# Kernel optimization log

Measured on AMD Instinct MI355X. Metric: run time of the kernel, lower is better.

The kernel has to match this reference:

```python
import jax, jax.numpy as jnp
import numpy as np
import math

B, C, F, W, NH = 2, 8, 1024, 512, 8
HD = F // NH


def conv2d(x, w, b):
    # NCHW 3x3 same-padding conv with bias
    y = jax.lax.conv_general_dilated(x, w, (1, 1), [(1, 1), (1, 1)],
                                     dimension_numbers=('NCHW', 'OIHW', 'NCHW'))
    return y + b[None, :, None, None]


def mc_linear(x, w):
    # per-channel linear over the feature (h) axis: (b,c,h,w) x (c,f,h) -> (b,c,f,w)
    return jnp.einsum('bchw,cfh->bcfw', x, w)


def split_heads(t):
    # (b,c,f,w) -> transpose(2,3) -> (b,c,w,f) -> (b,c,w,nh,hd) -> (b,c,nh,w,hd)
    b, c, f, w = t.shape
    return jnp.transpose(t.transpose(0, 1, 3, 2).reshape(b, c, w, NH, HD), (0, 1, 3, 2, 4))


def rotate_queries_or_keys(x):
    # lucidrains-style interleaved rotary over the sequence axis (dim -2)
    d, w = x.shape[-1], x.shape[-2]
    inv_freq = 1.0 / (10000.0 ** (jnp.arange(0, d, 2, dtype=jnp.float32) / d))
    freqs = jnp.arange(w, dtype=jnp.float32)[:, None] * inv_freq[None, :]  # (w, d/2)
    freqs = jnp.repeat(freqs, 2, axis=-1)  # (w, d)
    cos, sin = jnp.cos(freqs), jnp.sin(freqs)
    xp = x.reshape(*x.shape[:-1], d // 2, 2)
    x1, x2 = xp[..., 0], xp[..., 1]
    x_rot = jnp.stack((-x2, x1), axis=-1).reshape(x.shape)
    return x * cos + x_rot * sin


def _forward(x, prev_qk, wq_conv, bq_conv, wq_lin, wk_conv, bk_conv, wk_lin,
             wv_conv, bv_conv, wv_lin, wo_lin):
    b, c, h, w = x.shape
    q = rotate_queries_or_keys(split_heads(mc_linear(conv2d(x, wq_conv, bq_conv), wq_lin)))
    k = rotate_queries_or_keys(split_heads(mc_linear(conv2d(x, wk_conv, bk_conv), wk_lin)))
    v = split_heads(mc_linear(conv2d(x, wv_conv, bv_conv), wv_lin))
    # NOTE: original scales by sqrt(h) == sqrt(features), not sqrt(head_dim)
    qk = jnp.einsum('bcnqd,bcnkd->bcnqk', q, k) / math.sqrt(h) + prev_qk
    a = jnp.einsum('bcnqk,bcnkd->bcnqd', jax.nn.softmax(qk, axis=-1), v)
    a = jnp.transpose(a, (0, 1, 3, 2, 4)).reshape(b, c, w, h).transpose(0, 1, 3, 2)
    out = mc_linear(a, wo_lin)
    return out, qk


def setup_inputs() -> dict:
    key = jax.random.key(0)
    ks = jax.random.split(key, 10)
    s = 0.02
    return {
        'x': jax.random.normal(ks[0], (B, C, F, W), dtype=jnp.float32),
        'prev_qk': jax.random.normal(ks[1], (B, C, NH, W, W), dtype=jnp.float32) * 0.1,
        'wq_conv': jax.random.normal(ks[2], (C, C, 3, 3), dtype=jnp.float32) * s,
        'bq_conv': jnp.zeros((C,), dtype=jnp.float32),
        'wq_lin': jax.random.normal(ks[3], (C, F, F), dtype=jnp.float32) * s,
        'wk_conv': jax.random.normal(ks[4], (C, C, 3, 3), dtype=jnp.float32) * s,
        'bk_conv': jnp.zeros((C,), dtype=jnp.float32),
        'wk_lin': jax.random.normal(ks[5], (C, F, F), dtype=jnp.float32) * s,
        'wv_conv': jax.random.normal(ks[6], (C, C, 3, 3), dtype=jnp.float32) * s,
        'bv_conv': jnp.zeros((C,), dtype=jnp.float32),
        'wv_lin': jax.random.normal(ks[7], (C, F, F), dtype=jnp.float32) * s,
        'wo_lin': jax.random.normal(ks[8], (C, F, F), dtype=jnp.float32) * s,
    }


def reference(x, prev_qk, wq_conv, bq_conv, wq_lin, wk_conv, bk_conv, wk_lin,
              wv_conv, bv_conv, wv_lin, wo_lin):
    return _forward(x, prev_qk, wq_conv, bq_conv, wq_lin, wk_conv, bk_conv, wk_lin,
                    wv_conv, bv_conv, wv_lin, wo_lin)
```

## Files before the change

kernel.cpp:

```cpp
#include <hip/hip_runtime.h>
#include <stdint.h>


typedef float f32x4 __attribute__((ext_vector_type(4)));
typedef short s16x8 __attribute__((ext_vector_type(8)));

__device__ __forceinline__ short f2bf(float f) {
  union { float f; uint32_t u; } v; v.f = f;
  uint32_t r = v.u + 0x7FFFu + ((v.u >> 16) & 1u);
  return (short)(r >> 16);
}

__device__ __forceinline__ void g2l16(const void* g, void* l) {
  __builtin_amdgcn_global_load_lds(
      (const __attribute__((address_space(1))) void*)g,
      (__attribute__((address_space(3))) void*)l, 16, 0, 0);
}

__device__ __forceinline__ void gemm_core(const short* __restrict__ A,
                                          const short* __restrict__ B,
                                          int K, short* sA, short* sB,
                                          f32x4 (*acc)[4]) {
  const int tid = threadIdx.x;
  const int lane = tid & 63;
  const int wv = tid >> 6;
  const int wm = wv >> 1, wn = wv & 1;
  const int q = lane >> 4, cix = lane & 15;

  for (int k0 = 0; k0 < K; k0 += 32) {
    __syncthreads();
#pragma unroll
    for (int i = 0; i < 2; ++i) {
      int seg = wv + 4 * i;
      int m = seg * 16 + (lane >> 2);
      int ko = (lane & 3) * 8;
      g2l16(B + (size_t)m * K + k0 + ko, sB + seg * 512);
    }
#pragma unroll
    for (int i = 0; i < 2; ++i) {
      int seg = wv + 4 * i;
      int m = seg * 16 + (lane >> 2);
      int ko = (lane & 3) * 8;
      g2l16(A + (size_t)m * K + k0 + ko, sA + seg * 512);
    }
    __syncthreads();
    s16x8 afr[4], bfr[4];
#pragma unroll
    for (int i = 0; i < 4; ++i)
      afr[i] = *(const s16x8*)(sA + (wm * 64 + i * 16 + cix) * 32 + q * 8);
#pragma unroll
    for (int i = 0; i < 4; ++i)
      bfr[i] = *(const s16x8*)(sB + (wn * 64 + i * 16 + cix) * 32 + q * 8);
#pragma unroll
    for (int i = 0; i < 4; ++i)
#pragma unroll
      for (int j = 0; j < 4; ++j)
        acc[i][j] = __builtin_amdgcn_mfma_f32_16x16x32_bf16(afr[i], bfr[j],
                                                            acc[i][j], 0, 0, 0);
  }
}

__global__ void __launch_bounds__(256) k_cvt(
    const float* __restrict__ w0, const float* __restrict__ w1,
    const float* __restrict__ w2, const float* __restrict__ w3,
    short* __restrict__ Wb) {
  size_t i = (size_t)blockIdx.x * 256 + threadIdx.x;
#pragma unroll
  for (int r = 0; r < 4; ++r) {
    const float* s = (r == 0) ? w0 : (r == 1) ? w1 : (r == 2) ? w2 : w3;
    size_t v = i + (size_t)r * 2097152;
    float4 f = *(const float4*)(s + (i << 2));
    short4 o;
    o.x = f2bf(f.x); o.y = f2bf(f.y); o.z = f2bf(f.z); o.w = f2bf(f.w);
    *(short4*)(Wb + (v << 2)) = o;
  }
}

__global__ void __launch_bounds__(256) k_conv(
    const float* __restrict__ x,
    const float* __restrict__ wqc, const float* __restrict__ bqc,
    const float* __restrict__ wkc, const float* __restrict__ bkc,
    const float* __restrict__ wvc, const float* __restrict__ bvc,
    short* __restrict__ Yt) {
  __shared__ float xs[8][66][19];
  const int h0 = blockIdx.x * 64, w0 = blockIdx.y * 16, b = blockIdx.z;
  const int tid = threadIdx.x;
  for (int idx = tid; idx < 8 * 66 * 18; idx += 256) {
    int c = idx / (66 * 18);
    int rem = idx % (66 * 18);
    int r = rem / 18, cc = rem % 18;
    int h = h0 + r - 1, w = w0 + cc - 1;
    float v = 0.f;
    if (h >= 0 && h < 1024 && w >= 0 && w < 512)
      v = x[(((size_t)b * 8 + c) << 10 | (unsigned)h) * 512 + w];
    xs[c][r][cc] = v;
  }
  __syncthreads();
  const int hh = tid & 63;
  const int wv4 = tid >> 6;
  const size_t hgl = h0 + hh;
  for (int proj = 0; proj < 3; ++proj) {
    const float* wc = (proj == 0) ? wqc : ((proj == 1) ? wkc : wvc);
    const float* bc = (proj == 0) ? bqc : ((proj == 1) ? bkc : bvc);
    float a[4][8];
#pragma unroll
    for (int jj = 0; jj < 4; ++jj)
#pragma unroll
      for (int co = 0; co < 8; ++co) a[jj][co] = bc[co];
    for (int ci = 0; ci < 8; ++ci)
#pragma unroll
      for (int dh = 0; dh < 3; ++dh)
#pragma unroll
        for (int dw = 0; dw < 3; ++dw) {
          float xv[4];
#pragma unroll
          for (int jj = 0; jj < 4; ++jj)
            xv[jj] = xs[ci][hh + dh][wv4 * 4 + jj + dw];
          const int wi = ci * 9 + dh * 3 + dw;
#pragma unroll
          for (int co = 0; co < 8; ++co) {
            float wgt = wc[co * 72 + wi];
#pragma unroll
            for (int jj = 0; jj < 4; ++jj) a[jj][co] = fmaf(xv[jj], wgt, a[jj][co]);
          }
        }
#pragma unroll
    for (int jj = 0; jj < 4; ++jj) {
      size_t col = (size_t)b * 512 + w0 + wv4 * 4 + jj;
#pragma unroll
      for (int co = 0; co < 8; ++co)
        Yt[((size_t)(proj * 8 + co) << 20) + (col << 10) + hgl] = f2bf(a[jj][co]);
    }
  }
}

__global__ void __launch_bounds__(256) k_qkv(
    const short* __restrict__ Wb, const short* __restrict__ Yt,
    short* __restrict__ Qr, short* __restrict__ Kr, short* __restrict__ Vt) {
  __shared__ short sA[128 * 32], sB[128 * 32];
  const int L = blockIdx.x;
  const int lin = (L & 7) * 192 + (L >> 3);
  const int g = lin >> 6;
  const int t = lin & 63;
  const int proj = g >> 3, cq = g & 7;
  const int mt = t >> 3, nt = t & 7;
  const short* A = Wb + ((size_t)g << 20) + ((size_t)mt << 17);
  const short* B = Yt + ((size_t)g << 20) + ((size_t)nt << 17);
  const f32x4 fzero = {0.f, 0.f, 0.f, 0.f};
  f32x4 acc[4][4];
#pragma unroll
  for (int i = 0; i < 4; ++i)
#pragma unroll
    for (int j = 0; j < 4; ++j) acc[i][j] = fzero;
  gemm_core(A, B, 1024, sA, sB, acc);

  const int lane = threadIdx.x & 63, wv = threadIdx.x >> 6;
  const int wm = wv >> 1, wn = wv & 1, q = lane >> 4, cix = lane & 15;
  const int head = mt;
  if (proj == 2) {
#pragma unroll
    for (int mi = 0; mi < 4; ++mi) {
      int rbase = wm * 64 + mi * 16 + q * 4;
#pragma unroll
      for (int ni = 0; ni < 4; ++ni) {
        int col = nt * 128 + wn * 64 + ni * 16 + cix;
        int b = col >> 9, wpos = col & 511;
        size_t base = ((size_t)((cq * 8 + head) * 2 + b) << 16) +
                      ((size_t)rbase << 9) + wpos;
        f32x4 v = acc[mi][ni];
        Vt[base] = f2bf(v[0]);
        Vt[base + 512] = f2bf(v[1]);
        Vt[base + 1024] = f2bf(v[2]);
        Vt[base + 1536] = f2bf(v[3]);
      }
    }
  } else {
    short* QKp = proj ? Kr : Qr;
#pragma unroll
    for (int mi = 0; mi < 4; ++mi) {
      int rbase = wm * 64 + mi * 16 + q * 4;
      int j0 = rbase >> 1;
      float if0 = exp2f(-0.20762050593046f * (float)j0);
      float if1 = exp2f(-0.20762050593046f * (float)(j0 + 1));
#pragma unroll
      for (int ni = 0; ni < 4; ++ni) {
        int col = nt * 128 + wn * 64 + ni * 16 + cix;
        int b = col >> 9, wpos = col & 511;
        float fw = (float)wpos;
        float s0, c0, s1, c1;
        __sincosf(fw * if0, &s0, &c0);
        __sincosf(fw * if1, &s1, &c1);
        f32x4 v = acc[mi][ni];
        short4 pk;
        pk.x = f2bf(v[0] * c0 - v[1] * s0);
        pk.y = f2bf(v[1] * c0 + v[0] * s0);
        pk.z = f2bf(v[2] * c1 - v[3] * s1);
        pk.w = f2bf(v[3] * c1 + v[2] * s1);
        *(short4*)&QKp[((size_t)(((cq * 8 + head) * 2 + b) * 512 + wpos) << 7) +
                       rbase] = pk;
      }
    }
  }
}

__global__ void __launch_bounds__(256, 2) k_attn(
    const short* __restrict__ Qr, const short* __restrict__ Kr,
    const short* __restrict__ Vt, const float* __restrict__ prevqk,
    float* __restrict__ qk, short* __restrict__ At) {
  __shared__ short Qs[128 * 128];
  __shared__ short Pt[128 * 136];
  __shared__ float psum[128][2];
  const int tid = threadIdx.x, lane = tid & 63, wv = tid >> 6;
  const int wm = wv >> 1, wn = wv & 1, q = lane >> 4, cix = lane & 15;
  const int bid = blockIdx.x;
  const int lin = (bid & 7) * 64 + (bid >> 3);
  const int bcn = lin >> 2, qt = lin & 3;
  const int b = bcn >> 6, cch = (bcn >> 3) & 7, nh = bcn & 7;
  const size_t qrb = ((size_t)((cch * 8 + nh) * 2 + b)) << 16;
  const size_t rowg0 = (size_t)bcn * 512 + qt * 128;
  const int arow = wm * 64;

  {
    const char* Qg = (const char*)(Qr + qrb + ((size_t)qt << 14));
#pragma unroll
    for (int i = 0; i < 8; ++i) {
      int Lb = i * 4096 + wv * 1024;
      int L = Lb + (lane << 4);
      int src = (L & ~255) | ((L & 255) ^ (((L >> 8) & 15) << 4));
      g2l16(Qg + src, (char*)Qs + Lb);
    }
  }
  __syncthreads();

  const f32x4 fzero = {0.f, 0.f, 0.f, 0.f};
  f32x4 accO[4][4];
  float lsum[4][4];
#pragma unroll
  for (int i = 0; i < 4; ++i)
#pragma unroll
    for (int j = 0; j < 4; ++j) { accO[i][j] = fzero; lsum[i][j] = 0.f; }

  float pvA[16], pvB[16];

#pragma unroll 1
  for (int kt = 0; kt < 4; ++kt) {
    const int colb = kt * 128 + wn * 64 + cix;
    f32x4 accS[4][4];
#pragma unroll
    for (int i = 0; i < 4; ++i)
#pragma unroll
      for (int j = 0; j < 4; ++j) accS[i][j] = fzero;

#pragma unroll
    for (int ni = 0; ni < 4; ++ni)
#pragma unroll
      for (int r = 0; r < 4; ++r)
        pvA[ni * 4 + r] =
            prevqk[((rowg0 + arow + q * 4 + r) << 9) + colb + ni * 16];

    const short* Kbase = Kr + qrb + ((size_t)kt << 14);
#pragma unroll
    for (int kk = 0; kk < 4; ++kk) {
      s16x8 afr[4], bfr[4];
      const int cb = kk * 64 + q * 16;
#pragma unroll
      for (int ni = 0; ni < 4; ++ni)
        bfr[ni] = *(const s16x8*)(Kbase +
            ((size_t)(wn * 64 + ni * 16 + cix) << 7) + kk * 32 + q * 8);
#pragma unroll
      for (int mi = 0; mi < 4; ++mi) {
        const int row = arow + mi * 16 + cix;
        afr[mi] = *(const s16x8*)((const char*)Qs + row * 256 +
                                  (cb ^ ((row & 15) << 4)));
      }
      __builtin_amdgcn_s_setprio(1);
#pragma unroll
      for (int mi = 0; mi < 4; ++mi)
#pragma unroll
        for (int ni = 0; ni < 4; ++ni)
          accS[mi][ni] = __builtin_amdgcn_mfma_f32_16x16x32_bf16(
              afr[mi], bfr[ni], accS[mi][ni], 0, 0, 0);
      __builtin_amdgcn_s_setprio(0);
    }

    auto ldchunk = [&](int mi, float* dst) {
#pragma unroll
      for (int ni = 0; ni < 4; ++ni)
#pragma unroll
        for (int r = 0; r < 4; ++r)
          dst[ni * 4 + r] =
              prevqk[((rowg0 + arow + mi * 16 + q * 4 + r) << 9) +
                     colb + ni * 16];
    };
    auto process = [&](int mi, const float* pv) {
      float rs[4] = {0.f, 0.f, 0.f, 0.f};
#pragma unroll
      for (int ni = 0; ni < 4; ++ni)
#pragma unroll
        for (int r = 0; r < 4; ++r) {
          float s = accS[mi][ni][r] * 0.03125f + pv[ni * 4 + r];
          qk[((rowg0 + arow + mi * 16 + q * 4 + r) << 9) + colb + ni * 16] = s;
          float p = __expf(s);
          rs[r] += p;
          Pt[(arow + mi * 16 + q * 4 + r) * 136 + wn * 64 + ni * 16 + cix] =
              f2bf(p);
        }
#pragma unroll
      for (int r = 0; r < 4; ++r) lsum[mi][r] += rs[r];
    };
    ldchunk(1, pvB);
    process(0, pvA);
    ldchunk(2, pvA);
    process(1, pvB);
    ldchunk(3, pvB);
    process(2, pvA);
    process(3, pvB);

    __syncthreads();

#pragma unroll
    for (int s4 = 0; s4 < 4; ++s4) {
      s16x8 afr[4], bfr[4];
#pragma unroll
      for (int i = 0; i < 4; ++i)
        afr[i] =
            *(const s16x8*)&Pt[(arow + i * 16 + cix) * 136 + s4 * 32 + q * 8];
#pragma unroll
      for (int i = 0; i < 4; ++i)
        bfr[i] = *(const s16x8*)&Vt[qrb +
                                    ((size_t)(wn * 64 + i * 16 + cix) << 9) +
                                    kt * 128 + s4 * 32 + q * 8];
      __builtin_amdgcn_s_setprio(1);
#pragma unroll
      for (int i = 0; i < 4; ++i)
#pragma unroll
        for (int j = 0; j < 4; ++j)
          accO[i][j] = __builtin_amdgcn_mfma_f32_16x16x32_bf16(
              afr[i], bfr[j], accO[i][j], 0, 0, 0);
      __builtin_amdgcn_s_setprio(0);
    }
    __syncthreads();
  }

#pragma unroll
  for (int mi = 0; mi < 4; ++mi)
#pragma unroll
    for (int r = 0; r < 4; ++r) {
      float se = lsum[mi][r];
      se += __shfl_xor(se, 1);
      se += __shfl_xor(se, 2);
      se += __shfl_xor(se, 4);
      se += __shfl_xor(se, 8);
      if (cix == 0) psum[arow + mi * 16 + q * 4 + r][wn] = se;
    }
  __syncthreads();
#pragma unroll
  for (int mi = 0; mi < 4; ++mi) {
    int rl = arow + mi * 16 + q * 4;
    float iL[4];
#pragma unroll
    for (int r = 0; r < 4; ++r)
      iL[r] = 1.0f / (psum[rl + r][0] + psum[rl + r][1]);
    int wq = qt * 128 + rl;
#pragma unroll
    for (int ni = 0; ni < 4; ++ni) {
      int dl = wn * 64 + ni * 16 + cix;
      size_t ob = (((size_t)cch << 10) + b * 512 + wq) * 1024 + nh * 128 + dl;
      f32x4 v = accO[mi][ni];
      At[ob] = f2bf(v[0] * iL[0]);
      At[ob + 1024] = f2bf(v[1] * iL[1]);
      At[ob + 2048] = f2bf(v[2] * iL[2]);
      At[ob + 3072] = f2bf(v[3] * iL[3]);
    }
  }
}

__global__ void __launch_bounds__(256) k_out(
    const short* __restrict__ At, const short* __restrict__ Wob,
    float* __restrict__ outp) {
  __shared__ short sA[128 * 32], sB[128 * 32];
  const int L = blockIdx.x;
  const int lin = (L & 7) * 64 + (L >> 3);
  const int c = lin >> 6;
  const int t = lin & 63;
  const int mt = t >> 3, nt = t & 7;
  const short* A = At + ((size_t)c << 20) + ((size_t)mt << 17);
  const short* B = Wob + ((size_t)c << 20) + ((size_t)nt << 17);
  const f32x4 fzero = {0.f, 0.f, 0.f, 0.f};
  f32x4 acc[4][4];
#pragma unroll
  for (int i = 0; i < 4; ++i)
#pragma unroll
    for (int j = 0; j < 4; ++j) acc[i][j] = fzero;
  gemm_core(A, B, 1024, sA, sB, acc);

  const int lane = threadIdx.x & 63, wv = threadIdx.x >> 6;
  const int wm = wv >> 1, wn = wv & 1, q = lane >> 4, cix = lane & 15;
#pragma unroll
  for (int mi = 0; mi < 4; ++mi) {
    int colm = mt * 128 + wm * 64 + mi * 16 + q * 4;
    int b = colm >> 9, w = colm & 511;
#pragma unroll
    for (int ni = 0; ni < 4; ++ni) {
      int f = nt * 128 + wn * 64 + ni * 16 + cix;
      f32x4 v = acc[mi][ni];
      float4 st; st.x = v[0]; st.y = v[1]; st.z = v[2]; st.w = v[3];
      *(float4*)&outp[((((size_t)b * 8 + c) << 10) + f) * 512 + w] = st;
    }
  }
}

extern "C" void kernel_launch(void* const* d_in, const int* in_sizes, int n_in,
                              void* d_out, int out_size, void* d_ws,
                              size_t ws_size, hipStream_t stream) {
  const float* x = (const float*)d_in[0];
  const float* prevqk = (const float*)d_in[1];
  const float* wqc = (const float*)d_in[2];
  const float* bqc = (const float*)d_in[3];
  const float* wql = (const float*)d_in[4];
  const float* wkc = (const float*)d_in[5];
  const float* bkc = (const float*)d_in[6];
  const float* wkl = (const float*)d_in[7];
  const float* wvc = (const float*)d_in[8];
  const float* bvc = (const float*)d_in[9];
  const float* wvl = (const float*)d_in[10];
  const float* wol = (const float*)d_in[11];
  float* outp = (float*)d_out;
  float* qk = outp + 8388608;

  char* ws = (char*)d_ws;
  short* Wb = (short*)ws;
  short* Yt = (short*)(ws + 67108864);
  short* Qr = (short*)(ws + 117440512);
  short* Kr = (short*)(ws + 134217728);
  short* Vt = (short*)(ws + 150994944);
  short* At = (short*)(ws + 67108864);
  short* Wob = Wb + ((size_t)24 << 20);

  k_cvt<<<dim3(8192), 256, 0, stream>>>(wql, wkl, wvl, wol, Wb);
  k_conv<<<dim3(16, 32, 2), 256, 0, stream>>>(x, wqc, bqc, wkc, bkc, wvc, bvc, Yt);
  k_qkv<<<dim3(1536), 256, 0, stream>>>(Wb, Yt, Qr, Kr, Vt);
  k_attn<<<dim3(512), 256, 0, stream>>>(Qr, Kr, Vt, prevqk, qk, At);
  k_out<<<dim3(512), 256, 0, stream>>>(At, Wob, outp);
}
```

Measured before the change: 584.6 us.

## Double-buffer LDS tiles in GEMM core to overlap loads with MFMA

```diff
diff --git a/kernel.cpp b/kernel.cpp
--- a/kernel.cpp
+++ b/kernel.cpp
@@ -26,37 +26,48 @@
   const int wv = tid >> 6;
   const int wm = wv >> 1, wn = wv & 1;
   const int q = lane >> 4, cix = lane & 15;
-
-  for (int k0 = 0; k0 < K; k0 += 32) {
-    __syncthreads();
+  const int mrow = lane >> 2;
+  const int ko8 = (lane & 3) * 8;
+
+  auto stage = [&](int k0, int buf) {
+    short* dA = sA + buf * 4096;
+    short* dB = sB + buf * 4096;
 #pragma unroll
     for (int i = 0; i < 2; ++i) {
       int seg = wv + 4 * i;
-      int m = seg * 16 + (lane >> 2);
-      int ko = (lane & 3) * 8;
-      g2l16(B + (size_t)m * K + k0 + ko, sB + seg * 512);
+      int m = seg * 16 + mrow;
+      g2l16(B + (size_t)m * K + k0 + ko8, dB + seg * 512);
     }
 #pragma unroll
     for (int i = 0; i < 2; ++i) {
       int seg = wv + 4 * i;
-      int m = seg * 16 + (lane >> 2);
-      int ko = (lane & 3) * 8;
-      g2l16(A + (size_t)m * K + k0 + ko, sA + seg * 512);
-    }
-    __syncthreads();
+      int m = seg * 16 + mrow;
+      g2l16(A + (size_t)m * K + k0 + ko8, dA + seg * 512);
+    }
+  };
+
+  stage(0, 0);
+  __syncthreads();
+  int buf = 0;
+  for (int k0 = 0; k0 < K; k0 += 32) {
+    if (k0 + 32 < K) stage(k0 + 32, buf ^ 1);
+    const short* cA = sA + buf * 4096;
+    const short* cB = sB + buf * 4096;
     s16x8 afr[4], bfr[4];
 #pragma unroll
     for (int i = 0; i < 4; ++i)
-      afr[i] = *(const s16x8*)(sA + (wm * 64 + i * 16 + cix) * 32 + q * 8);
+      afr[i] = *(const s16x8*)(cA + (wm * 64 + i * 16 + cix) * 32 + q * 8);
 #pragma unroll
     for (int i = 0; i < 4; ++i)
-      bfr[i] = *(const s16x8*)(sB + (wn * 64 + i * 16 + cix) * 32 + q * 8);
+      bfr[i] = *(const s16x8*)(cB + (wn * 64 + i * 16 + cix) * 32 + q * 8);
 #pragma unroll
     for (int i = 0; i < 4; ++i)
 #pragma unroll
       for (int j = 0; j < 4; ++j)
         acc[i][j] = __builtin_amdgcn_mfma_f32_16x16x32_bf16(afr[i], bfr[j],
                                                             acc[i][j], 0, 0, 0);
+    __syncthreads();
+    buf ^= 1;
   }
 }
 
@@ -137,7 +148,7 @@
 __global__ void __launch_bounds__(256) k_qkv(
     const short* __restrict__ Wb, const short* __restrict__ Yt,
     short* __restrict__ Qr, short* __restrict__ Kr, short* __restrict__ Vt) {
-  __shared__ short sA[128 * 32], sB[128 * 32];
+  __shared__ short sA[2 * 128 * 32], sB[2 * 128 * 32];
   const int L = blockIdx.x;
   const int lin = (L & 7) * 192 + (L >> 3);
   const int g = lin >> 6;
@@ -378,7 +389,7 @@
 __global__ void __launch_bounds__(256) k_out(
     const short* __restrict__ At, const short* __restrict__ Wob,
     float* __restrict__ outp) {
-  __shared__ short sA[128 * 32], sB[128 * 32];
+  __shared__ short sA[2 * 128 * 32], sB[2 * 128 * 32];
   const int L = blockIdx.x;
   const int lin = (L & 7) * 64 + (L >> 3);
   const int c = lin >> 6;
```

Measured after the change: 578.2 us. About the same (-1.1%).
